# Performance work log

Measured on AMD Instinct MI355X. Metric: run time of the kernel, lower is better.

Reference implementation:

```python
import jax, jax.numpy as jnp
import numpy as np
import math

B, N, H, L, P = 128, 512, 512, 256, 3
T = N - 1  # decode steps t = 1..N-1


def setup_inputs() -> dict:
    key = jax.random.key(0)
    ks = jax.random.split(key, 24)
    s = 0.02
    rn = lambda k, shape: jax.random.normal(k, shape, jnp.float32) * s
    # valid tree parents: parent[0] = -1, parent[t] in [0, t)
    raw = jax.random.randint(ks[0], (B, N), 0, N)
    t_idx = jnp.arange(N)[None, :]
    parent = jnp.where(t_idx == 0, -1, raw % jnp.maximum(t_idx, 1)).astype(jnp.int32)
    return {
        'z': jax.random.normal(ks[1], (B, L), jnp.float32),
        'target_pos': jax.random.normal(ks[2], (B, N, P), jnp.float32),
        'W_zh': rn(ks[3], (H, L)), 'b_zh': jnp.zeros((H,), jnp.float32),
        'W_ne': rn(ks[4], (H, P + 1)), 'b_ne': jnp.zeros((H,), jnp.float32),
        'W_ih': rn(ks[5], (3 * H, H)), 'b_ih': jnp.zeros((3 * H,), jnp.float32),
        'W_hh': rn(ks[6], (3 * H, H)), 'b_hh': jnp.zeros((3 * H,), jnp.float32),
        'W_q': rn(ks[7], (H, H)), 'b_q': jnp.zeros((H,), jnp.float32),
        'W_k': rn(ks[8], (H, H)), 'b_k': jnp.zeros((H,), jnp.float32),
        'W_mu': rn(ks[9], (P, 2 * H)), 'b_mu': jnp.zeros((P,), jnp.float32),
        'W_lv': rn(ks[10], (P, 2 * H)), 'b_lv': jnp.zeros((P,), jnp.float32),
        'W_s': rn(ks[11], (1, H)), 'b_s': jnp.zeros((1,), jnp.float32),
        'parent': parent,
    }


def _forward(z, target_pos, W_zh, b_zh, W_ne, b_ne, W_ih, b_ih, W_hh, b_hh,
             W_q, b_q, W_k, b_k, W_mu, b_mu, W_lv, b_lv, W_s, b_s, parent):
    # root position is zeros; nodes t>=1 use teacher-forced target positions
    pos_full = target_pos.at[:, 0, :].set(0.0)  # [B,N,P]
    # NB: original code always feeds child_count = 0 into node_encoder
    feat = jnp.concatenate([pos_full, jnp.zeros(pos_full.shape[:-1] + (1,), pos_full.dtype)], -1)
    embeds = feat @ W_ne.T + b_ne  # [B,N,H]

    h0 = jnp.tanh(z @ W_zh.T + b_zh)  # [B,H]
    # precompute GRU input projections for steps t=1..N-1 (input = embeds[t-1])
    Xp = embeds[:, :T] @ W_ih.T + b_ih  # [B,T,3H]

    def gru_step(h, xp):
        hp = h @ W_hh.T + b_hh
        xr, xu, xn = jnp.split(xp, 3, axis=-1)
        hr, hu, hn = jnp.split(hp, 3, axis=-1)
        r = jax.nn.sigmoid(xr + hr)
        u = jax.nn.sigmoid(xu + hu)
        n = jnp.tanh(xn + r * hn)
        h2 = (1.0 - u) * n + u * h
        return h2, h2

    _, Hs = jax.lax.scan(gru_step, h0, jnp.swapaxes(Xp, 0, 1))  # [T,B,H]
    Hs = jnp.swapaxes(Hs, 0, 1)  # [B,T,H]; Hs[:,i] = h at step t=i+1

    # attention over the first t nodes (causal mask replaces the growing stack)
    Q = Hs @ W_q.T + b_q            # [B,T,H]
    K = embeds @ W_k.T + b_k        # [B,N,H]
    logits = jnp.einsum('bth,bnh->btn', Q, K) / math.sqrt(H)
    valid_key = jnp.arange(N)[None, :] <= jnp.arange(T)[:, None]  # key j < t=i+1
    logits = jnp.where(valid_key[None, :, :], logits, -1e9)
    logp = jax.nn.log_softmax(logits, axis=-1)

    tp = parent[:, 1:]  # true parent for t=1..N-1, [B,T]
    tp_valid = (tp >= 0) & (tp < jnp.arange(1, N)[None, :])
    tp_safe = jnp.clip(tp, 0, N - 1)
    ce = -jnp.take_along_axis(logp, tp_safe[:, :, None], axis=-1)[..., 0]
    loss_parent = jnp.where(tp_valid, ce, 0.0).sum(-1) / T

    chosen = jnp.maximum(tp, 0)  # teacher-forced parent (clamped)
    gather = jax.vmap(lambda a, i: a[i])
    parent_embed = gather(embeds, chosen)   # [B,T,H]
    parent_pos = gather(pos_full, chosen)   # [B,T,P]

    pos_in = jnp.concatenate([Hs, parent_embed], axis=-1)  # [B,T,2H]
    mu = pos_in @ W_mu.T + b_mu
    logvar = pos_in @ W_lv.T + b_lv
    off = target_pos[:, 1:] - parent_pos
    pos_nll = 0.5 * (logvar + (off - mu) ** 2 / (jnp.exp(logvar) + 1e-8))
    loss_pos = pos_nll.sum((1, 2)) / T

    stop_logit = (Hs @ W_s.T + b_s)[..., 0]  # [B,T]
    labels = jnp.zeros((T,), jnp.float32).at[-1].set(1.0)  # is_last
    bce = labels * jax.nn.softplus(-stop_logit) + (1.0 - labels) * jax.nn.softplus(stop_logit)
    loss_stop = bce.sum(-1) / T

    return jnp.stack([loss_parent, loss_pos, loss_stop], axis=-1)  # [B,3]


def reference(z, target_pos, W_zh, b_zh, W_ne, b_ne, W_ih, b_ih, W_hh, b_hh,
              W_q, b_q, W_k, b_k, W_mu, b_mu, W_lv, b_lv, W_s, b_s, parent):
    return _forward(z, target_pos, W_zh, b_zh, W_ne, b_ne, W_ih, b_ih, W_hh, b_hh,
                    W_q, b_q, W_k, b_k, W_mu, b_mu, W_lv, b_lv, W_s, b_s, parent)
```

## Files before the change

### kernel.cpp

```cpp
#include <hip/hip_runtime.h>
#include <cstdint>
#include <cstddef>

typedef unsigned short u16;
typedef short bf16x8 __attribute__((ext_vector_type(8)));
typedef float f32x4 __attribute__((ext_vector_type(4)));

union F16B { float4 f; f32x4 fv; bf16x8 v; u16 u[8]; };
union U4 { f32x4 f; uint32_t u[4]; };

#define SENT 0x7FC07FC0u

__device__ __forceinline__ u16 f2b(float f) {
  uint32_t x = __float_as_uint(f);
  return (u16)((x + 0x7FFFu + ((x >> 16) & 1u)) >> 16);
}
__device__ __forceinline__ float b2f(u16 h) { return __uint_as_float(((uint32_t)h) << 16); }
__device__ __forceinline__ float sigm(float x) { return 1.0f / (1.0f + __expf(-x)); }
__device__ __forceinline__ float tanh_(float x) { return 1.0f - 2.0f / (__expf(2.0f * x) + 1.0f); }
__device__ __forceinline__ float splus(float x) { return logf(1.0f + __expf(x)); }
__device__ __forceinline__ bf16x8 asbf(f32x4 x) { F16B u; u.fv = x; return u.v; }
__device__ __forceinline__ uint32_t umin_(uint32_t a, uint32_t b) { return a < b ? a : b; }

__device__ __forceinline__ void llc_st128(u16* p, f32x4 v) {
  asm volatile("global_store_dwordx4 %0, %1, off sc0 sc1" :: "v"(p), "v"(v) : "memory");
}

constexpr size_t OFF_AIH   = 32768;
constexpr size_t OFF_CIH   = 57344;
constexpr size_t OFF_AK    = 63488;
constexpr size_t OFF_CK    = 71680;
constexpr size_t OFF_AMU2  = 73728;
constexpr size_t OFF_CMU2  = 73792;
constexpr size_t OFF_ALV2  = 73856;
constexpr size_t OFF_CLV2  = 73920;
constexpr size_t OFF_WHH   = 336128;
constexpr size_t OFF_WQ    = 1908992;
constexpr size_t OFF_KF    = 2433280;
constexpr size_t OFF_QF    = 69542144;
constexpr size_t OFF_RING  = OFF_QF;
constexpr size_t OFF_HS    = 136651008;

__global__ void k_zero(float* out, uint32_t* ring32) {
  int tid = blockIdx.x * 1024 + threadIdx.x;
  if (tid < 384) out[tid] = 0.f;
  ring32[32768 + tid] = SENT;
}

__global__ void k_fold(const float* __restrict__ Wih, const float* __restrict__ bih,
                       const float* __restrict__ Wk,  const float* __restrict__ bk,
                       const float* __restrict__ Wmu, const float* __restrict__ bmu,
                       const float* __restrict__ Wlv, const float* __restrict__ blv,
                       const float* __restrict__ Wne, const float* __restrict__ bne,
                       float* Aih, float* cih, float* Ak, float* ck,
                       float* Amu2, float* cmu2, float* Alv2, float* clv2) {
  int tid = blockIdx.x * 256 + threadIdx.x;
  if (tid >= 2054 * 5) return;
  int row = tid / 5, c = tid % 5;
  const float* wrow; float bias; float* Adst; float* cdst;
  if (row < 1536)      { wrow = Wih + (size_t)row * 512;              bias = bih[row];      Adst = Aih  + row * 4;        cdst = cih  + row; }
  else if (row < 2048) { int j = row - 1536; wrow = Wk + (size_t)j * 512;       bias = bk[j];  Adst = Ak   + j * 4; cdst = ck   + j; }
  else if (row < 2051) { int j = row - 2048; wrow = Wmu + (size_t)j * 1024 + 512; bias = bmu[j]; Adst = Amu2 + j * 4; cdst = cmu2 + j; }
  else                 { int j = row - 2051; wrow = Wlv + (size_t)j * 1024 + 512; bias = blv[j]; Adst = Alv2 + j * 4; cdst = clv2 + j; }
  float acc = 0.f;
  if (c < 4) { for (int h = 0; h < 512; ++h) acc += wrow[h] * Wne[h * 4 + c]; Adst[c] = acc; }
  else       { for (int h = 0; h < 512; ++h) acc += wrow[h] * bne[h];         cdst[0] = bias + acc; }
}

__global__ void k_h0(const float* __restrict__ z, const float* __restrict__ Wzh,
                     const float* __restrict__ bzh, u16* __restrict__ ring) {
  int tid = blockIdx.x * 256 + threadIdx.x;
  int row = tid >> 6, ug = tid & 63;
  const float* zr = z + row * 256;
  F16B o;
  #pragma unroll
  for (int e = 0; e < 8; ++e) {
    int u = ug * 8 + e;
    float acc = bzh[u];
    const float* wr = Wzh + (size_t)u * 256;
    for (int k = 0; k < 256; ++k) acc += zr[k] * wr[k];
    o.u[e] = f2b(tanh_(acc));
  }
  int rt = row >> 4, kt = ug >> 2, sub = ug & 3;
  int lane = sub * 16 + (row & 15);
  *(float4*)(ring + (size_t)(((rt * 16 + kt) * 64 + lane) * 8)) = o.f;
}

__global__ void k_wcvt(const float* __restrict__ W, u16* __restrict__ dst, int ntiles) {
  int tid = blockIdx.x * 256 + threadIdx.x;
  if (tid >= ntiles * 1024) return;
  int rem = tid & 1023, l = rem & 63;
  int nt = tid >> 10, kt = rem >> 6;
  int row = nt * 16 + (l & 15);
  int kb = kt * 32 + (l >> 4) * 8;
  const float* src = W + (size_t)row * 512 + kb;
  F16B o;
  #pragma unroll
  for (int e = 0; e < 8; ++e) o.u[e] = f2b(src[e]);
  *(float4*)(dst + (size_t)tid * 8) = o.f;
}

__global__ void k_kfrag(const float* __restrict__ tpos, const float* __restrict__ Ak,
                        const float* __restrict__ ck, u16* __restrict__ Kf) {
  int tid = blockIdx.x * 256 + threadIdx.x;
  int b = tid >> 15, rem = tid & 32767;
  int r2 = rem & 1023, l = r2 & 63;
  int nt = rem >> 10, kt = r2 >> 6;
  int n = nt * 16 + (l & 15);
  int kb = kt * 32 + (l >> 4) * 8;
  float f0 = 0.f, f1 = 0.f, f2 = 0.f;
  if (n > 0) { const float* fp = tpos + ((size_t)b * 512 + n) * 3; f0 = fp[0]; f1 = fp[1]; f2 = fp[2]; }
  F16B o;
  #pragma unroll
  for (int e = 0; e < 8; ++e) {
    int hh = kb + e;
    o.u[e] = f2b(ck[hh] + f0 * Ak[hh * 4] + f1 * Ak[hh * 4 + 1] + f2 * Ak[hh * 4 + 2]);
  }
  *(float4*)(Kf + (size_t)tid * 8) = o.f;
}

__global__ __launch_bounds__(256, 1) void k_gru(
    const float* __restrict__ tpos, const float* __restrict__ Aih, const float* __restrict__ cih,
    const float* __restrict__ bhh, const u16* __restrict__ whh,
    u16* __restrict__ ring, u16* __restrict__ Hs) {
  const int bid = blockIdx.x;
  const int half = bid & 1;
  const int g = bid >> 1;
  const int tid = threadIdx.x;
  const int w = tid >> 6;
  const int l = tid & 63;
  const int fl = l & 15, fh = l >> 4;
  __shared__ F16B wsm[3072];
  __shared__ __align__(16) u16 trn[4][384];

  {
    const float4* src = (const float4*)whh;
    #pragma unroll
    for (int it = 0; it < 12; ++it) {
      int i = it * 256 + tid;
      int ntl = i >> 10;
      int rem = i & 1023;
      int gnt = (ntl == 0) ? g : (ntl == 1 ? 32 + g : 64 + g);
      wsm[i].f = src[(size_t)gnt * 1024 + rem];
    }
  }
  const int jj = (g << 4) + fl;
  const float Ar0 = Aih[jj*4], Ar1 = Aih[jj*4+1], Ar2 = Aih[jj*4+2];
  const float Au0 = Aih[(512+jj)*4], Au1 = Aih[(512+jj)*4+1], Au2 = Aih[(512+jj)*4+2];
  const float An0 = Aih[(1024+jj)*4], An1 = Aih[(1024+jj)*4+1], An2 = Aih[(1024+jj)*4+2];
  const float cr = cih[jj] + bhh[jj];
  const float cu = cih[512+jj] + bhh[512+jj];
  const float cn = cih[1024+jj];
  const float bhn = bhh[1024+jj];
  const int rowbase = half * 64 + (w << 4);
  const int rt = (half << 2) + w;

  float hprev[4];
  {
    int kt_h = g >> 1;
    int sub_h = ((g & 1) << 1) | (fl >> 3);
    int e_h = fl & 7;
    #pragma unroll
    for (int i = 0; i < 4; ++i) {
      int lr = (fh << 2) + i;
      hprev[i] = b2f(ring[(size_t)(((rt * 16 + kt_h) * 64 + sub_h * 16 + lr) * 8 + e_h)]);
    }
  }
  const int cl = fl;
  const int cs = fh & 1;
  u16* Tw = &trn[w][0];
  u16* rdst_base = ring + ((size_t)(rt * 16 + (g >> 1)) * 64 + ((((g & 1) << 1) | cs) * 16 + cl)) * 8;
  const u16* abase0 = ring + ((size_t)(rt * 16) * 64 + l) * 8;
  f32x4 sentv;
  sentv[0] = sentv[1] = sentv[2] = sentv[3] = __uint_as_float(SENT);
  __syncthreads();

  int cur = 0;
  for (int t = 0; t < 511; ++t) {
    int wr = cur + 1;  if (wr == 3) wr = 0;
    int clr = wr + 1;  if (clr == 3) clr = 0;

    float f0[4], f1[4], f2[4];
    #pragma unroll
    for (int i = 0; i < 4; ++i) {
      f0[i] = 0.f; f1[i] = 0.f; f2[i] = 0.f;
      if (t > 0) {
        const float* fp = tpos + ((size_t)(rowbase + (fh << 2) + i) * 512 + t) * 3;
        f0[i] = fp[0]; f1[i] = fp[1]; f2[i] = fp[2];
      }
    }

    const u16* b0 = abase0 + ((size_t)cur << 16);
    const u16* b1 = b0 + 2048;
    const u16* b2 = b0 + 4096;
    const u16* b3 = b0 + 6144;
    f32x4 a0,a1,a2,a3,a4,a5,a6,a7,a8,a9,a10,a11,a12,a13,a14,a15;
    while (true) {
      asm volatile(
        "global_load_dwordx4 %0, %16, off sc0 sc1\n\t"
        "global_load_dwordx4 %1, %16, off offset:1024 sc0 sc1\n\t"
        "global_load_dwordx4 %2, %16, off offset:2048 sc0 sc1\n\t"
        "global_load_dwordx4 %3, %16, off offset:3072 sc0 sc1\n\t"
        "global_load_dwordx4 %4, %17, off sc0 sc1\n\t"
        "global_load_dwordx4 %5, %17, off offset:1024 sc0 sc1\n\t"
        "global_load_dwordx4 %6, %17, off offset:2048 sc0 sc1\n\t"
        "global_load_dwordx4 %7, %17, off offset:3072 sc0 sc1\n\t"
        "global_load_dwordx4 %8, %18, off sc0 sc1\n\t"
        "global_load_dwordx4 %9, %18, off offset:1024 sc0 sc1\n\t"
        "global_load_dwordx4 %10, %18, off offset:2048 sc0 sc1\n\t"
        "global_load_dwordx4 %11, %18, off offset:3072 sc0 sc1\n\t"
        "global_load_dwordx4 %12, %19, off sc0 sc1\n\t"
        "global_load_dwordx4 %13, %19, off offset:1024 sc0 sc1\n\t"
        "global_load_dwordx4 %14, %19, off offset:2048 sc0 sc1\n\t"
        "global_load_dwordx4 %15, %19, off offset:3072 sc0 sc1\n\t"
        "s_waitcnt vmcnt(0)"
        : "=&v"(a0),"=&v"(a1),"=&v"(a2),"=&v"(a3),"=&v"(a4),"=&v"(a5),"=&v"(a6),"=&v"(a7),
          "=&v"(a8),"=&v"(a9),"=&v"(a10),"=&v"(a11),"=&v"(a12),"=&v"(a13),"=&v"(a14),"=&v"(a15)
        : "v"(b0),"v"(b1),"v"(b2),"v"(b3)
        : "memory");
      __builtin_amdgcn_sched_barrier(0);
      uint32_t mn = 0xFFFFFFFFu;
#define CHK(R) { U4 x; x.f = (R); \
      mn = umin_(mn, x.u[0]^SENT); mn = umin_(mn, x.u[1]^SENT); \
      mn = umin_(mn, x.u[2]^SENT); mn = umin_(mn, x.u[3]^SENT); }
      CHK(a0) CHK(a1) CHK(a2) CHK(a3) CHK(a4) CHK(a5) CHK(a6) CHK(a7)
      CHK(a8) CHK(a9) CHK(a10) CHK(a11) CHK(a12) CHK(a13) CHK(a14) CHK(a15)
#undef CHK
      if (__ballot(mn == 0u) == 0ull) break;
    }
    __builtin_amdgcn_sched_barrier(0);

    if (l < 32) llc_st128(rdst_base + ((size_t)clr << 16), sentv);

    f32x4 x0 = {0.f,0.f,0.f,0.f}, x1 = {0.f,0.f,0.f,0.f}, x2 = {0.f,0.f,0.f,0.f};
    f32x4 y0 = {0.f,0.f,0.f,0.f}, y1 = {0.f,0.f,0.f,0.f}, y2 = {0.f,0.f,0.f,0.f};
#define GRU_STEP(A, KT, A0, A1, A2) { bf16x8 av = asbf(A); \
    A0 = __builtin_amdgcn_mfma_f32_16x16x32_bf16(av, wsm[(0*16+(KT))*64 + l].v, A0, 0, 0, 0); \
    A1 = __builtin_amdgcn_mfma_f32_16x16x32_bf16(av, wsm[(1*16+(KT))*64 + l].v, A1, 0, 0, 0); \
    A2 = __builtin_amdgcn_mfma_f32_16x16x32_bf16(av, wsm[(2*16+(KT))*64 + l].v, A2, 0, 0, 0); }
    GRU_STEP(a0,0,x0,x1,x2)   GRU_STEP(a8,8,y0,y1,y2)
    GRU_STEP(a1,1,x0,x1,x2)   GRU_STEP(a9,9,y0,y1,y2)
    GRU_STEP(a2,2,x0,x1,x2)   GRU_STEP(a10,10,y0,y1,y2)
    GRU_STEP(a3,3,x0,x1,x2)   GRU_STEP(a11,11,y0,y1,y2)
    GRU_STEP(a4,4,x0,x1,x2)   GRU_STEP(a12,12,y0,y1,y2)
    GRU_STEP(a5,5,x0,x1,x2)   GRU_STEP(a13,13,y0,y1,y2)
    GRU_STEP(a6,6,x0,x1,x2)   GRU_STEP(a14,14,y0,y1,y2)
    GRU_STEP(a7,7,x0,x1,x2)   GRU_STEP(a15,15,y0,y1,y2)
#undef GRU_STEP
    f32x4 acc0 = x0 + y0, acc1 = x1 + y1, acc2 = x2 + y2;

    #pragma unroll
    for (int i = 0; i < 4; ++i) {
      float rr = sigm(cr + f0[i] * Ar0 + f1[i] * Ar1 + f2[i] * Ar2 + acc0[i]);
      float uu = sigm(cu + f0[i] * Au0 + f1[i] * Au1 + f2[i] * Au2 + acc1[i]);
      float nn = tanh_(cn + f0[i] * An0 + f1[i] * An1 + f2[i] * An2 + rr * (acc2[i] + bhn));
      float h2 = (1.f - uu) * nn + uu * hprev[i];
      hprev[i] = h2;
      Tw[((fh << 2) + i) * 24 + fl] = f2b(h2);
    }
    asm volatile("s_waitcnt lgkmcnt(0)" ::: "memory");
    __builtin_amdgcn_sched_barrier(0);

    f32x4 chunk = *(const f32x4*)(Tw + cl * 24 + cs * 8);
    if (l < 32) llc_st128(rdst_base + ((size_t)wr << 16), chunk);
    if (l >= 32)
      *(f32x4*)(Hs + ((size_t)(rowbase + cl) * 511 + t) * 512 + (g << 4) + cs * 8) = chunk;

    cur = wr;
  }
}

__global__ __launch_bounds__(256) void k_qgemm(const u16* __restrict__ Hs, const u16* __restrict__ wq,
                                               const float* __restrict__ bq, u16* __restrict__ Qf) {
  const int bid0 = blockIdx.x;
  const int bid = (bid0 & 7) * 512 + (bid0 >> 3);
  const int b = bid >> 5, mt = bid & 31;
  const int tid = threadIdx.x, w = tid >> 6, l = tid & 63;
  const int fl = l & 15, fh = l >> 4;
  __shared__ float qsm[16 * 516];
  int t = mt * 16 + fl; if (t > 510) t = 510;
  const u16* arow = Hs + ((size_t)b * 511 + t) * 512 + fh * 8;
  f32x4 acc[8];
  #pragma unroll
  for (int p = 0; p < 8; ++p) acc[p] = (f32x4){0.f,0.f,0.f,0.f};
  for (int kt = 0; kt < 16; ++kt) {
    F16B a; a.f = *(const float4*)(arow + kt * 32);
    #pragma unroll
    for (int p = 0; p < 8; ++p) {
      F16B bb; bb.f = *(const float4*)(wq + ((size_t)((w * 8 + p) * 16 + kt) * 64 + l) * 8);
      acc[p] = __builtin_amdgcn_mfma_f32_16x16x32_bf16(a.v, bb.v, acc[p], 0, 0, 0);
    }
  }
  #pragma unroll
  for (int p = 0; p < 8; ++p) {
    int n = (w * 8 + p) * 16 + fl;
    float add = bq[n];
    #pragma unroll
    for (int i = 0; i < 4; ++i)
      qsm[(fh * 4 + i) * 516 + n] = acc[p][i] + add;
  }
  __syncthreads();
  #pragma unroll
  for (int q = 0; q < 4; ++q) {
    int kt = w * 4 + q;
    const float* src = &qsm[fl * 516 + kt * 32 + fh * 8];
    F16B o;
    #pragma unroll
    for (int e = 0; e < 8; ++e) o.u[e] = f2b(src[e]);
    *(float4*)(Qf + (((size_t)(b * 32 + mt) * 16 + kt) * 64 + l) * 8) = o.f;
  }
}

__global__ __launch_bounds__(256) void k_attn(const u16* __restrict__ Qf, const u16* __restrict__ Kf,
                                              const int* __restrict__ parent, float* __restrict__ out) {
  const int bid0 = blockIdx.x;
  const int bid = (bid0 & 7) * 512 + (bid0 >> 3);
  const int b = bid >> 5, mt = bid & 31;
  const int tid = threadIdx.x, w = tid >> 6, l = tid & 63;
  const int fl = l & 15, fh = l >> 4;
  __shared__ float sm_m[4][16], sm_s[4][16], sm_t[16];
  f32x4 acc[8];
  #pragma unroll
  for (int p = 0; p < 8; ++p) acc[p] = (f32x4){0.f,0.f,0.f,0.f};
  for (int kt = 0; kt < 16; ++kt) {
    F16B a; a.f = *(const float4*)(Qf + (((size_t)(b * 32 + mt) * 16 + kt) * 64 + l) * 8);
    #pragma unroll
    for (int p = 0; p < 8; ++p) {
      int nt = w + 4 * p;
      if (nt <= mt) {
        F16B bb; bb.f = *(const float4*)(Kf + (((size_t)(b * 32 + nt) * 16 + kt) * 64 + l) * 8);
        acc[p] = __builtin_amdgcn_mfma_f32_16x16x32_bf16(a.v, bb.v, acc[p], 0, 0, 0);
      }
    }
  }
  const float scale = 0.044194173824159216f;
  float S[8][4];
  float mrow[4] = {-3e38f, -3e38f, -3e38f, -3e38f};
  #pragma unroll
  for (int p = 0; p < 8; ++p) {
    int nt = w + 4 * p;
    int n = nt * 16 + fl;
    #pragma unroll
    for (int i = 0; i < 4; ++i) {
      int t = mt * 16 + fh * 4 + i;
      float s = -1e9f;
      if (nt <= mt && n <= t) s = acc[p][i] * scale;
      S[p][i] = s;
      mrow[i] = fmaxf(mrow[i], s);
    }
  }
  #pragma unroll
  for (int i = 0; i < 4; ++i) {
    #pragma unroll
    for (int off = 1; off < 16; off <<= 1)
      mrow[i] = fmaxf(mrow[i], __shfl_xor(mrow[i], off, 64));
  }
  if (fl == 0) {
    #pragma unroll
    for (int i = 0; i < 4; ++i) sm_m[w][fh * 4 + i] = mrow[i];
  }
  __syncthreads();
  float M[4], esum[4];
  #pragma unroll
  for (int i = 0; i < 4; ++i) {
    int r = fh * 4 + i;
    M[i] = fmaxf(fmaxf(sm_m[0][r], sm_m[1][r]), fmaxf(sm_m[2][r], sm_m[3][r]));
    esum[i] = 0.f;
  }
  #pragma unroll
  for (int i = 0; i < 4; ++i) {
    int t = mt * 16 + fh * 4 + i;
    int tp = (t < 511) ? parent[b * 512 + t + 1] : -1;
    #pragma unroll
    for (int p = 0; p < 8; ++p) {
      int nt = w + 4 * p;
      int n = nt * 16 + fl;
      float e = (nt <= mt) ? __expf(S[p][i] - M[i]) : 0.f;
      esum[i] += e;
      if (nt <= mt && n == tp) sm_t[fh * 4 + i] = S[p][i];
    }
  }
  #pragma unroll
  for (int i = 0; i < 4; ++i) {
    #pragma unroll
    for (int off = 1; off < 16; off <<= 1)
      esum[i] += __shfl_xor(esum[i], off, 64);
  }
  if (fl == 0) {
    #pragma unroll
    for (int i = 0; i < 4; ++i) sm_s[w][fh * 4 + i] = esum[i];
  }
  __syncthreads();
  if (tid < 16) {
    int r = tid, t = mt * 16 + r;
    if (t < 511) {
      int tp = parent[b * 512 + t + 1];
      if (tp >= 0 && tp <= t) {
        float Mv = fmaxf(fmaxf(sm_m[0][r], sm_m[1][r]), fmaxf(sm_m[2][r], sm_m[3][r]));
        float Sv = sm_s[0][r] + sm_s[1][r] + sm_s[2][r] + sm_s[3][r];
        float ce = Mv + logf(Sv) - sm_t[r];
        atomicAdd(&out[b * 3 + 0], ce * (1.0f / 511.0f));
      }
    }
  }
}

__global__ __launch_bounds__(256) void k_pos(const u16* __restrict__ Hs, const float* __restrict__ tpos,
    const int* __restrict__ parent, const float* __restrict__ Wmu, const float* __restrict__ Wlv,
    const float* __restrict__ Ws, const float* __restrict__ bs,
    const float* __restrict__ Amu2, const float* __restrict__ cmu2,
    const float* __restrict__ Alv2, const float* __restrict__ clv2,
    float* __restrict__ out) {
  const int l = threadIdx.x & 63;
  int wid = blockIdx.x * 4 + (threadIdx.x >> 6);
  const int nw = gridDim.x * 4;
  for (int idx = wid; idx < 128 * 511; idx += nw) {
    int b = idx / 511, t = idx - b * 511;
    const u16* hrow = Hs + ((size_t)b * 511 + t) * 512 + l * 8;
    float h[8];
    #pragma unroll
    for (int e = 0; e < 8; ++e) h[e] = b2f(hrow[e]);
    float d0=0,d1=0,d2=0,d3=0,d4=0,d5=0,d6=0;
    #pragma unroll
    for (int e = 0; e < 8; ++e) {
      int c = l * 8 + e;
      d0 += h[e] * Wmu[c]; d1 += h[e] * Wmu[1024 + c]; d2 += h[e] * Wmu[2048 + c];
      d3 += h[e] * Wlv[c]; d4 += h[e] * Wlv[1024 + c]; d5 += h[e] * Wlv[2048 + c];
      d6 += h[e] * Ws[c];
    }
    #pragma unroll
    for (int off = 32; off; off >>= 1) {
      d0 += __shfl_xor(d0, off); d1 += __shfl_xor(d1, off); d2 += __shfl_xor(d2, off);
      d3 += __shfl_xor(d3, off); d4 += __shfl_xor(d4, off); d5 += __shfl_xor(d5, off);
      d6 += __shfl_xor(d6, off);
    }
    if (l == 0) {
      int tp = parent[b * 512 + t + 1];
      int ch = tp > 0 ? tp : 0;
      float p0 = 0.f, p1 = 0.f, p2 = 0.f;
      if (ch > 0) { const float* pp = tpos + ((size_t)b * 512 + ch) * 3; p0 = pp[0]; p1 = pp[1]; p2 = pp[2]; }
      const float* op = tpos + ((size_t)b * 512 + t + 1) * 3;
      float dm[3] = {d0, d1, d2}, dl[3] = {d3, d4, d5};
      float nll = 0.f;
      #pragma unroll
      for (int p = 0; p < 3; ++p) {
        float pc = (p == 0) ? p0 : (p == 1 ? p1 : p2);
        float mu = dm[p] + cmu2[p] + p0 * Amu2[p*4] + p1 * Amu2[p*4+1] + p2 * Amu2[p*4+2];
        float lv = dl[p] + clv2[p] + p0 * Alv2[p*4] + p1 * Alv2[p*4+1] + p2 * Alv2[p*4+2];
        float dd = (op[p] - pc) - mu;
        nll += 0.5f * (lv + dd * dd / (__expf(lv) + 1e-8f));
      }
      float sl = d6 + bs[0];
      float bce = (t == 510) ? splus(-sl) : splus(sl);
      atomicAdd(&out[b * 3 + 1], nll * (1.0f / 511.0f));
      atomicAdd(&out[b * 3 + 2], bce * (1.0f / 511.0f));
    }
  }
}

extern "C" void kernel_launch(void* const* d_in, const int* in_sizes, int n_in,
                              void* d_out, int out_size, void* d_ws, size_t ws_size,
                              hipStream_t stream) {
  const float* z    = (const float*)d_in[0];
  const float* tpos = (const float*)d_in[1];
  const float* Wzh  = (const float*)d_in[2];
  const float* bzh  = (const float*)d_in[3];
  const float* Wne  = (const float*)d_in[4];
  const float* bne  = (const float*)d_in[5];
  const float* Wih  = (const float*)d_in[6];
  const float* bih  = (const float*)d_in[7];
  const float* Whh  = (const float*)d_in[8];
  const float* bhh  = (const float*)d_in[9];
  const float* Wq   = (const float*)d_in[10];
  const float* bq   = (const float*)d_in[11];
  const float* Wk   = (const float*)d_in[12];
  const float* bk   = (const float*)d_in[13];
  const float* Wmu  = (const float*)d_in[14];
  const float* bmu  = (const float*)d_in[15];
  const float* Wlv  = (const float*)d_in[16];
  const float* blv  = (const float*)d_in[17];
  const float* Ws   = (const float*)d_in[18];
  const float* bs   = (const float*)d_in[19];
  const int*   par  = (const int*)d_in[20];
  float* out = (float*)d_out;
  char* ws = (char*)d_ws;

  float* Aih   = (float*)(ws + OFF_AIH);
  float* cih   = (float*)(ws + OFF_CIH);
  float* Ak    = (float*)(ws + OFF_AK);
  float* ck    = (float*)(ws + OFF_CK);
  float* Amu2  = (float*)(ws + OFF_AMU2);
  float* cmu2  = (float*)(ws + OFF_CMU2);
  float* Alv2  = (float*)(ws + OFF_ALV2);
  float* clv2  = (float*)(ws + OFF_CLV2);
  u16*   ring  = (u16*)(ws + OFF_RING);
  u16*   whhf  = (u16*)(ws + OFF_WHH);
  u16*   wqf   = (u16*)(ws + OFF_WQ);
  u16*   Kf    = (u16*)(ws + OFF_KF);
  u16*   Qf    = (u16*)(ws + OFF_QF);
  u16*   Hs    = (u16*)(ws + OFF_HS);
  (void)ws_size; (void)in_sizes; (void)n_in; (void)out_size;

  hipLaunchKernelGGL(k_zero,  dim3(64),    dim3(1024), 0, stream, out, (uint32_t*)ring);
  hipLaunchKernelGGL(k_fold,  dim3(41),    dim3(256), 0, stream, Wih, bih, Wk, bk, Wmu, bmu, Wlv, blv, Wne, bne,
                     Aih, cih, Ak, ck, Amu2, cmu2, Alv2, clv2);
  hipLaunchKernelGGL(k_h0,    dim3(32),    dim3(256), 0, stream, z, Wzh, bzh, ring);
  hipLaunchKernelGGL(k_wcvt,  dim3(128),   dim3(256), 0, stream, Wq, wqf, 32);
  hipLaunchKernelGGL(k_wcvt,  dim3(384),   dim3(256), 0, stream, Whh, whhf, 96);
  hipLaunchKernelGGL(k_kfrag, dim3(16384), dim3(256), 0, stream, tpos, Ak, ck, Kf);
  hipLaunchKernelGGL(k_gru,   dim3(64),    dim3(256), 0, stream, tpos, Aih, cih, bhh, whhf, ring, Hs);
  hipLaunchKernelGGL(k_qgemm, dim3(4096),  dim3(256), 0, stream, Hs, wqf, bq, Qf);
  hipLaunchKernelGGL(k_attn,  dim3(4096),  dim3(256), 0, stream, Qf, Kf, par, out);
  hipLaunchKernelGGL(k_pos,   dim3(512),   dim3(256), 0, stream, Hs, tpos, par, Wmu, Wlv, Ws, bs,
                     Amu2, cmu2, Alv2, clv2, out);
}
```

Measured before the change: 2.222 ms.

## Fuse Q projection, attention loss, and position/stop heads into one kernel

```diff
diff --git a/kernel.cpp b/kernel.cpp
--- a/kernel.cpp
+++ b/kernel.cpp
@@ -270,27 +270,78 @@
   }
 }
 
-__global__ __launch_bounds__(256) void k_qgemm(const u16* __restrict__ Hs, const u16* __restrict__ wq,
-                                               const float* __restrict__ bq, u16* __restrict__ Qf) {
+__global__ __launch_bounds__(256) void k_qattn(
+    const u16* __restrict__ Hs, const u16* __restrict__ wq, const float* __restrict__ bq,
+    const u16* __restrict__ Kf, const int* __restrict__ parent,
+    const float* __restrict__ tpos,
+    const float* __restrict__ Wmu, const float* __restrict__ Wlv,
+    const float* __restrict__ Ws, const float* __restrict__ bs,
+    const float* __restrict__ Amu2, const float* __restrict__ cmu2,
+    const float* __restrict__ Alv2, const float* __restrict__ clv2,
+    float* __restrict__ out) {
   const int bid0 = blockIdx.x;
   const int bid = (bid0 & 7) * 512 + (bid0 >> 3);
   const int b = bid >> 5, mt = bid & 31;
   const int tid = threadIdx.x, w = tid >> 6, l = tid & 63;
   const int fl = l & 15, fh = l >> 4;
   __shared__ float qsm[16 * 516];
-  int t = mt * 16 + fl; if (t > 510) t = 510;
-  const u16* arow = Hs + ((size_t)b * 511 + t) * 512 + fh * 8;
+  __shared__ float sm_m[4][16], sm_s[4][16], sm_t[16];
+
+  const int t0 = mt * 16 + fl;
+  const int tq = t0 > 510 ? 510 : t0;
+  const u16* arow = Hs + ((size_t)b * 511 + tq) * 512 + fh * 8;
   f32x4 acc[8];
   #pragma unroll
   for (int p = 0; p < 8; ++p) acc[p] = (f32x4){0.f,0.f,0.f,0.f};
+  float d0=0,d1=0,d2=0,d3=0,d4=0,d5=0,d6=0;
   for (int kt = 0; kt < 16; ++kt) {
     F16B a; a.f = *(const float4*)(arow + kt * 32);
+    if (w == 0) {
+      int c = kt * 32 + fh * 8;
+      #pragma unroll
+      for (int e = 0; e < 8; ++e) {
+        float hv = b2f(a.u[e]);
+        d0 += hv * Wmu[c+e]; d1 += hv * Wmu[1024+c+e]; d2 += hv * Wmu[2048+c+e];
+        d3 += hv * Wlv[c+e]; d4 += hv * Wlv[1024+c+e]; d5 += hv * Wlv[2048+c+e];
+        d6 += hv * Ws[c+e];
+      }
+    }
     #pragma unroll
     for (int p = 0; p < 8; ++p) {
       F16B bb; bb.f = *(const float4*)(wq + ((size_t)((w * 8 + p) * 16 + kt) * 64 + l) * 8);
       acc[p] = __builtin_amdgcn_mfma_f32_16x16x32_bf16(a.v, bb.v, acc[p], 0, 0, 0);
     }
   }
+  if (w == 0) {
+    d0 += __shfl_xor(d0, 16); d0 += __shfl_xor(d0, 32);
+    d1 += __shfl_xor(d1, 16); d1 += __shfl_xor(d1, 32);
+    d2 += __shfl_xor(d2, 16); d2 += __shfl_xor(d2, 32);
+    d3 += __shfl_xor(d3, 16); d3 += __shfl_xor(d3, 32);
+    d4 += __shfl_xor(d4, 16); d4 += __shfl_xor(d4, 32);
+    d5 += __shfl_xor(d5, 16); d5 += __shfl_xor(d5, 32);
+    d6 += __shfl_xor(d6, 16); d6 += __shfl_xor(d6, 32);
+    if (fh == 0 && t0 < 511) {
+      int tp = parent[b * 512 + t0 + 1];
+      int ch = tp > 0 ? tp : 0;
+      float p0 = 0.f, p1 = 0.f, p2 = 0.f;
+      if (ch > 0) { const float* pp = tpos + ((size_t)b * 512 + ch) * 3; p0 = pp[0]; p1 = pp[1]; p2 = pp[2]; }
+      const float* op = tpos + ((size_t)b * 512 + t0 + 1) * 3;
+      float dm[3] = {d0, d1, d2}, dl[3] = {d3, d4, d5};
+      float nll = 0.f;
+      #pragma unroll
+      for (int p = 0; p < 3; ++p) {
+        float pc = (p == 0) ? p0 : (p == 1 ? p1 : p2);
+        float mu = dm[p] + cmu2[p] + p0 * Amu2[p*4] + p1 * Amu2[p*4+1] + p2 * Amu2[p*4+2];
+        float lv = dl[p] + clv2[p] + p0 * Alv2[p*4] + p1 * Alv2[p*4+1] + p2 * Alv2[p*4+2];
+        float dd = (op[p] - pc) - mu;
+        nll += 0.5f * (lv + dd * dd / (__expf(lv) + 1e-8f));
+      }
+      float sl = d6 + bs[0];
+      float bce = (t0 == 510) ? splus(-sl) : splus(sl);
+      atomicAdd(&out[b * 3 + 1], nll * (1.0f / 511.0f));
+      atomicAdd(&out[b * 3 + 2], bce * (1.0f / 511.0f));
+    }
+  }
   #pragma unroll
   for (int p = 0; p < 8; ++p) {
     int n = (w * 8 + p) * 16 + fl;
@@ -300,36 +351,21 @@
       qsm[(fh * 4 + i) * 516 + n] = acc[p][i] + add;
   }
   __syncthreads();
-  #pragma unroll
-  for (int q = 0; q < 4; ++q) {
-    int kt = w * 4 + q;
+
+  f32x4 att[8];
+  #pragma unroll
+  for (int p = 0; p < 8; ++p) att[p] = (f32x4){0.f,0.f,0.f,0.f};
+  for (int kt = 0; kt < 16; ++kt) {
     const float* src = &qsm[fl * 516 + kt * 32 + fh * 8];
-    F16B o;
-    #pragma unroll
-    for (int e = 0; e < 8; ++e) o.u[e] = f2b(src[e]);
-    *(float4*)(Qf + (((size_t)(b * 32 + mt) * 16 + kt) * 64 + l) * 8) = o.f;
-  }
-}
-
-__global__ __launch_bounds__(256) void k_attn(const u16* __restrict__ Qf, const u16* __restrict__ Kf,
-                                              const int* __restrict__ parent, float* __restrict__ out) {
-  const int bid0 = blockIdx.x;
-  const int bid = (bid0 & 7) * 512 + (bid0 >> 3);
-  const int b = bid >> 5, mt = bid & 31;
-  const int tid = threadIdx.x, w = tid >> 6, l = tid & 63;
-  const int fl = l & 15, fh = l >> 4;
-  __shared__ float sm_m[4][16], sm_s[4][16], sm_t[16];
-  f32x4 acc[8];
-  #pragma unroll
-  for (int p = 0; p < 8; ++p) acc[p] = (f32x4){0.f,0.f,0.f,0.f};
-  for (int kt = 0; kt < 16; ++kt) {
-    F16B a; a.f = *(const float4*)(Qf + (((size_t)(b * 32 + mt) * 16 + kt) * 64 + l) * 8);
+    F16B a;
+    #pragma unroll
+    for (int e = 0; e < 8; ++e) a.u[e] = f2b(src[e]);
     #pragma unroll
     for (int p = 0; p < 8; ++p) {
       int nt = w + 4 * p;
       if (nt <= mt) {
         F16B bb; bb.f = *(const float4*)(Kf + (((size_t)(b * 32 + nt) * 16 + kt) * 64 + l) * 8);
-        acc[p] = __builtin_amdgcn_mfma_f32_16x16x32_bf16(a.v, bb.v, acc[p], 0, 0, 0);
+        att[p] = __builtin_amdgcn_mfma_f32_16x16x32_bf16(a.v, bb.v, att[p], 0, 0, 0);
       }
     }
   }
@@ -344,7 +380,7 @@
     for (int i = 0; i < 4; ++i) {
       int t = mt * 16 + fh * 4 + i;
       float s = -1e9f;
-      if (nt <= mt && n <= t) s = acc[p][i] * scale;
+      if (nt <= mt && n <= t) s = att[p][i] * scale;
       S[p][i] = s;
       mrow[i] = fmaxf(mrow[i], s);
     }
@@ -401,59 +437,6 @@
         float ce = Mv + logf(Sv) - sm_t[r];
         atomicAdd(&out[b * 3 + 0], ce * (1.0f / 511.0f));
       }
-    }
-  }
-}
-
-__global__ __launch_bounds__(256) void k_pos(const u16* __restrict__ Hs, const float* __restrict__ tpos,
-    const int* __restrict__ parent, const float* __restrict__ Wmu, const float* __restrict__ Wlv,
-    const float* __restrict__ Ws, const float* __restrict__ bs,
-    const float* __restrict__ Amu2, const float* __restrict__ cmu2,
-    const float* __restrict__ Alv2, const float* __restrict__ clv2,
-    float* __restrict__ out) {
-  const int l = threadIdx.x & 63;
-  int wid = blockIdx.x * 4 + (threadIdx.x >> 6);
-  const int nw = gridDim.x * 4;
-  for (int idx = wid; idx < 128 * 511; idx += nw) {
-    int b = idx / 511, t = idx - b * 511;
-    const u16* hrow = Hs + ((size_t)b * 511 + t) * 512 + l * 8;
-    float h[8];
-    #pragma unroll
-    for (int e = 0; e < 8; ++e) h[e] = b2f(hrow[e]);
-    float d0=0,d1=0,d2=0,d3=0,d4=0,d5=0,d6=0;
-    #pragma unroll
-    for (int e = 0; e < 8; ++e) {
-      int c = l * 8 + e;
-      d0 += h[e] * Wmu[c]; d1 += h[e] * Wmu[1024 + c]; d2 += h[e] * Wmu[2048 + c];
-      d3 += h[e] * Wlv[c]; d4 += h[e] * Wlv[1024 + c]; d5 += h[e] * Wlv[2048 + c];
-      d6 += h[e] * Ws[c];
-    }
-    #pragma unroll
-    for (int off = 32; off; off >>= 1) {
-      d0 += __shfl_xor(d0, off); d1 += __shfl_xor(d1, off); d2 += __shfl_xor(d2, off);
-      d3 += __shfl_xor(d3, off); d4 += __shfl_xor(d4, off); d5 += __shfl_xor(d5, off);
-      d6 += __shfl_xor(d6, off);
-    }
-    if (l == 0) {
-      int tp = parent[b * 512 + t + 1];
-      int ch = tp > 0 ? tp : 0;
-      float p0 = 0.f, p1 = 0.f, p2 = 0.f;
-      if (ch > 0) { const float* pp = tpos + ((size_t)b * 512 + ch) * 3; p0 = pp[0]; p1 = pp[1]; p2 = pp[2]; }
-      const float* op = tpos + ((size_t)b * 512 + t + 1) * 3;
-      float dm[3] = {d0, d1, d2}, dl[3] = {d3, d4, d5};
-      float nll = 0.f;
-      #pragma unroll
-      for (int p = 0; p < 3; ++p) {
-        float pc = (p == 0) ? p0 : (p == 1 ? p1 : p2);
-        float mu = dm[p] + cmu2[p] + p0 * Amu2[p*4] + p1 * Amu2[p*4+1] + p2 * Amu2[p*4+2];
-        float lv = dl[p] + clv2[p] + p0 * Alv2[p*4] + p1 * Alv2[p*4+1] + p2 * Alv2[p*4+2];
-        float dd = (op[p] - pc) - mu;
-        nll += 0.5f * (lv + dd * dd / (__expf(lv) + 1e-8f));
-      }
-      float sl = d6 + bs[0];
-      float bce = (t == 510) ? splus(-sl) : splus(sl);
-      atomicAdd(&out[b * 3 + 1], nll * (1.0f / 511.0f));
-      atomicAdd(&out[b * 3 + 2], bce * (1.0f / 511.0f));
     }
   }
 }
@@ -497,7 +480,6 @@
   u16*   whhf  = (u16*)(ws + OFF_WHH);
   u16*   wqf   = (u16*)(ws + OFF_WQ);
   u16*   Kf    = (u16*)(ws + OFF_KF);
-  u16*   Qf    = (u16*)(ws + OFF_QF);
   u16*   Hs    = (u16*)(ws + OFF_HS);
   (void)ws_size; (void)in_sizes; (void)n_in; (void)out_size;
 
@@ -509,8 +491,6 @@
   hipLaunchKernelGGL(k_wcvt,  dim3(384),   dim3(256), 0, stream, Whh, whhf, 96);
   hipLaunchKernelGGL(k_kfrag, dim3(16384), dim3(256), 0, stream, tpos, Ak, ck, Kf);
   hipLaunchKernelGGL(k_gru,   dim3(64),    dim3(256), 0, stream, tpos, Aih, cih, bhh, whhf, ring, Hs);
-  hipLaunchKernelGGL(k_qgemm, dim3(4096),  dim3(256), 0, stream, Hs, wqf, bq, Qf);
-  hipLaunchKernelGGL(k_attn,  dim3(4096),  dim3(256), 0, stream, Qf, Kf, par, out);
-  hipLaunchKernelGGL(k_pos,   dim3(512),   dim3(256), 0, stream, Hs, tpos, par, Wmu, Wlv, Ws, bs,
-                     Amu2, cmu2, Alv2, clv2, out);
-}
+  hipLaunchKernelGGL(k_qattn, dim3(4096),  dim3(256), 0, stream, Hs, wqf, bq, Kf, par, tpos,
+                     Wmu, Wlv, Ws, bs, Amu2, cmu2, Alv2, clv2, out);
+}
```

New measurement: 1.933 ms, median of 2. -13.0%, faster.
